# Kernel tuning notes

Hardware: AMD Instinct MI355X
Metric: run time of the kernel (lower is better)

## Reference

```python
import jax, jax.numpy as jnp
import numpy as np

S, B, H, E, V, L = 256, 32, 2000, 512, 10000, 6
EPS = 1e-5

def bn(x, g, b, m, v):
    # eval-mode batch norm over last (feature) dim
    return g * (x - m) * jax.lax.rsqrt(v + EPS) + b

def indrnn(x, u):
    # x: [S, B, F], u: [F]; h_t = relu(x_t + u * h_{t-1})
    def step(h, xt):
        h = jax.nn.relu(xt + u * h)
        return h, h
    h0 = jnp.zeros(x.shape[1:], x.dtype)
    _, ys = jax.lax.scan(step, h0, x)
    return ys

def setup_inputs():
    key = jax.random.key(0)
    ks = jax.random.split(key, 16)
    inp = {}
    inp['tokens'] = jax.random.randint(ks[0], (S, B), 0, V)
    inp['emb'] = jax.random.uniform(ks[1], (V, E), jnp.float32, -0.01, 0.01)
    inp['W0'] = jax.random.normal(ks[2], (E, H), jnp.float32) * (1.0 / np.sqrt(E))
    inp['b0'] = jnp.zeros((H,), jnp.float32)
    inp['Wr'] = jax.random.normal(ks[3], (L - 1, H, H), jnp.float32) * (1.0 / np.sqrt(H))
    inp['br'] = jnp.zeros((L - 1, H), jnp.float32)
    inp['u'] = jax.random.uniform(ks[4], (L, H), jnp.float32, 0.0, 1.0)
    inp['g'] = jnp.ones((L, H), jnp.float32)
    inp['be'] = jnp.zeros((L, H), jnp.float32)
    inp['mu'] = jnp.zeros((L, H), jnp.float32)
    inp['var'] = jnp.ones((L, H), jnp.float32)
    inp['Wl'] = jax.random.normal(ks[5], (H, E), jnp.float32) * (1.0 / np.sqrt(H))
    inp['bl'] = jnp.zeros((E,), jnp.float32)
    inp['ul'] = jax.random.uniform(ks[6], (E,), jnp.float32, 0.0, 1.0)
    inp['gl'] = jnp.ones((E,), jnp.float32)
    inp['bel'] = jnp.zeros((E,), jnp.float32)
    inp['mul'] = jnp.zeros((E,), jnp.float32)
    inp['varl'] = jnp.ones((E,), jnp.float32)
    inp['g2'] = jnp.ones((E,), jnp.float32)
    inp['be2'] = jnp.zeros((E,), jnp.float32)
    inp['mu2'] = jnp.zeros((E,), jnp.float32)
    inp['var2'] = jnp.ones((E,), jnp.float32)
    inp['Wd'] = jax.random.uniform(ks[7], (E, V), jnp.float32, -0.01, 0.01)
    inp['bd'] = jnp.zeros((V,), jnp.float32)
    return inp

def reference(tokens, emb, W0, b0, Wr, br, u, g, be, mu, var,
              Wl, bl, ul, gl, bel, mul, varl, g2, be2, mu2, var2, Wd, bd):
    x = emb[tokens]  # [S, B, E]
    # dropout layers are identity in eval mode
    for l in range(L):
        if l == 0:
            x = jnp.einsum('sbe,eh->sbh', x, W0) + b0
        else:
            x = jnp.einsum('sbh,hk->sbk', x, Wr[l - 1]) + br[l - 1]
        x = bn(x, g[l], be[l], mu[l], var[l])   # bn_before
        x = indrnn(x, u[l])
    x = jnp.einsum('sbh,he->sbe', x, Wl) + bl   # last_fc
    x = bn(x, gl, bel, mul, varl)
    x = indrnn(x, ul)                            # last_indrnn
    x = bn(x, g2, be2, mu2, var2)                # extra_bn (bn_before mode)
    out = (jnp.einsum('sbe,ev->sbv', x, Wd) + bd).reshape(S * B, V)
    return out
```

## Files before the change

kernel.cpp:

```cpp
#include <hip/hip_runtime.h>
#include <hip/hip_bf16.h>

#define S_LEN  256
#define BATCH  32
#define SB     8192
#define EDIM   512
#define HDIM   2000
#define HP     2048
#define VDIM   10000
#define VP     10240
#define EPS_BN 1e-5f


typedef __attribute__((ext_vector_type(8))) short bfx8;
typedef __attribute__((ext_vector_type(4))) float f32x4;

__device__ __forceinline__ void gload_lds16(const void* g, void* l) {
  __builtin_amdgcn_global_load_lds(
      (const __attribute__((address_space(1))) void*)g,
      (__attribute__((address_space(3))) void*)l, 16, 0, 0);
}

__device__ __forceinline__ float bf_lo(unsigned int w) {
  return __builtin_bit_cast(float, (unsigned int)(w << 16));
}
__device__ __forceinline__ float bf_hi(unsigned int w) {
  return __builtin_bit_cast(float, (unsigned int)(w & 0xFFFF0000u));
}
__device__ __forceinline__ unsigned int bf_pack(float lo, float hi) {
  unsigned short a = __builtin_bit_cast(unsigned short, __float2bfloat16(lo));
  unsigned short b = __builtin_bit_cast(unsigned short, __float2bfloat16(hi));
  return (unsigned int)a | ((unsigned int)b << 16);
}

#define PREP_GRID 29788
__global__ __launch_bounds__(256) void prep_kernel(
    const float* __restrict__ W0, const float* __restrict__ Wr,
    const float* __restrict__ Wl, const float* __restrict__ Wd,
    __hip_bfloat16* __restrict__ wt0, __hip_bfloat16* __restrict__ wtr,
    __hip_bfloat16* __restrict__ wtl, __hip_bfloat16* __restrict__ wtd,
    const float* __restrict__ b0, const float* __restrict__ br,
    const float* __restrict__ g,  const float* __restrict__ be,
    const float* __restrict__ mu, const float* __restrict__ var,
    const float* __restrict__ bl, const float* __restrict__ gl,
    const float* __restrict__ bel,const float* __restrict__ mul_,
    const float* __restrict__ varl,
    const float* __restrict__ g2, const float* __restrict__ be2,
    const float* __restrict__ mu2,const float* __restrict__ var2,
    const float* __restrict__ bd,
    float* es, float* eh, float* fs, float* fh,
    float* s2, float* h2, float* ds, float* dh,
    const int* __restrict__ tokens, const float* __restrict__ emb,
    __hip_bfloat16* __restrict__ xb) {
  __shared__ float tile[32][33];
  const int id = blockIdx.x;
  const int t = threadIdx.x;

  if (id < 27648) {
    const float* W; __hip_bfloat16* Wt; int K, N, Kp, Np, bx, by;
    if (id < 1024) {
      W = W0; Wt = wt0; K = EDIM; N = HDIM; Kp = EDIM; Np = HP;
      bx = id & 15; by = id >> 4;
    } else if (id < 21504) {
      int rel = id - 1024; int l = rel >> 12; int r2 = rel & 4095;
      W = Wr + (size_t)l * HDIM * HDIM; Wt = wtr + (size_t)l * HP * HP;
      K = HDIM; N = HDIM; Kp = HP; Np = HP;
      bx = r2 & 63; by = r2 >> 6;
    } else if (id < 22528) {
      int rel = id - 21504;
      W = Wl; Wt = wtl; K = HDIM; N = EDIM; Kp = HP; Np = EDIM;
      bx = rel & 63; by = rel >> 6;
    } else {
      int rel = id - 22528;
      W = Wd; Wt = wtd; K = EDIM; N = VDIM; Kp = EDIM; Np = VP;
      bx = rel & 15; by = rel >> 4;
    }
    const int tx = t & 31, ty = t >> 5;
    const int kb = bx * 32, nb = by * 32;
#pragma unroll
    for (int i = 0; i < 4; i++) {
      int k = kb + ty + i * 8, n = nb + tx;
      tile[ty + i * 8][tx] = (k < K && n < N) ? W[(size_t)k * N + n] : 0.f;
    }
    __syncthreads();
#pragma unroll
    for (int i = 0; i < 4; i++) {
      int n = nb + ty + i * 8, k = kb + tx;
      if (n < Np && k < Kp) Wt[(size_t)n * Kp + k] = __float2bfloat16(tile[tx][ty + i * 8]);
    }
    return;
  }

  if (id < 27740) {
    int tt = (id - 27648) * 256 + t;
    if (tt < 6 * HP) {
      int l = tt >> 11, h = tt & (HP - 1);
      float sc = 0.f, sh = 0.f;
      if (h < HDIM) {
        float s = g[l * HDIM + h] * rsqrtf(var[l * HDIM + h] + EPS_BN);
        float bias = (l == 0) ? b0[h] : br[(l - 1) * HDIM + h];
        sc = s;
        sh = (bias - mu[l * HDIM + h]) * s + be[l * HDIM + h];
      }
      es[tt] = sc; eh[tt] = sh;
      return;
    }
    tt -= 6 * HP;
    if (tt < EDIM) {
      float s = gl[tt] * rsqrtf(varl[tt] + EPS_BN);
      fs[tt] = s; fh[tt] = (bl[tt] - mul_[tt]) * s + bel[tt];
      return;
    }
    tt -= EDIM;
    if (tt < EDIM) {
      float s = g2[tt] * rsqrtf(var2[tt] + EPS_BN);
      s2[tt] = s; h2[tt] = be2[tt] - mu2[tt] * s;
      return;
    }
    tt -= EDIM;
    if (tt < VP) {
      ds[tt] = 1.f; dh[tt] = (tt < VDIM) ? bd[tt] : 0.f;
    }
    return;
  }

  {
    int idx = (id - 27740) * 256 + t;
    int mprime = idx >> 6;
    int e0 = (idx & 63) << 3;
    int s = mprime & 255, b = mprime >> 8;
    int tok = tokens[s * BATCH + b];
    const float* src = emb + (size_t)tok * EDIM + e0;
    float4 v0 = ((const float4*)src)[0];
    float4 v1 = ((const float4*)src)[1];
    __hip_bfloat16 tmp[8];
    tmp[0] = __float2bfloat16(v0.x); tmp[1] = __float2bfloat16(v0.y);
    tmp[2] = __float2bfloat16(v0.z); tmp[3] = __float2bfloat16(v0.w);
    tmp[4] = __float2bfloat16(v1.x); tmp[5] = __float2bfloat16(v1.y);
    tmp[6] = __float2bfloat16(v1.z); tmp[7] = __float2bfloat16(v1.w);
    *(bfx8*)&xb[(size_t)mprime * EDIM + e0] = *(const bfx8*)tmp;
  }
}

#define BARX  __builtin_amdgcn_s_barrier()
#define SP1   __builtin_amdgcn_s_setprio(1)
#define SP0   __builtin_amdgcn_s_setprio(0)
#define LGKM0 do { asm volatile("s_waitcnt lgkmcnt(0)" ::: "memory"); \
                   __builtin_amdgcn_sched_barrier(0); } while (0)
#define VMC(n) asm volatile("s_waitcnt vmcnt(" #n ")" ::: "memory")

__global__ __launch_bounds__(512, 2) void gemm256p_bf16_kernel(
    const __hip_bfloat16* __restrict__ A, int lda,
    const __hip_bfloat16* __restrict__ Bt, int ldb,
    __hip_bfloat16* __restrict__ Cb, float* __restrict__ Cf, int ldc,
    const float* __restrict__ epS, const float* __restrict__ epH,
    const float* __restrict__ uscan,
    int Kp, int Nstore, int grid_m, int chunk2d) {
  __shared__ __align__(16) char smem[131072];
  const int t = threadIdx.x, lane = t & 63, wid = t >> 6;
  const int nwg = gridDim.x, q = nwg >> 3, wg = blockIdx.x;
  int bm, bn;
  if (chunk2d) {
    const int xc = wg & 7, i = wg >> 3;
    bm = xc * 4 + (i >> 3);
    bn = i & 7;
  } else {
    const int swzb = (wg & 7) * q + (wg >> 3);
    bm = swzb % grid_m; bn = swzb / grid_m;
  }
  const int m0 = bm * 256, n0 = bn * 256;
  const int wm = wid >> 2, wn = wid & 3;

  const int lrow = lane >> 3;
  const int lch  = ((lane & 7) ^ lrow) * 8;
  const __hip_bfloat16* gA = A  + (size_t)(m0 + wid * 8 + lrow) * lda + lch;
  const __hip_bfloat16* gB = Bt + (size_t)(n0 + (wid >> 2) * 64 + (wid & 3) * 8 + lrow) * ldb + lch;
  char* const ldsA = (char*)smem;
  char* const ldsB = (char*)smem + 65536;
  const int laoff = wid * 1024;
  const int lboff = (wid >> 2) * 8192 + (wid & 3) * 1024;

#define STA(buf, e, kt) do {                                                   \
    gload_lds16(gA + (size_t)((e) * 64) * lda + (kt) * 64,                     \
                ldsA + (buf) * 32768 + (e) * 8192 + laoff);                    \
    gload_lds16(gA + (size_t)(128 + (e) * 64) * lda + (kt) * 64,               \
                ldsA + (buf) * 32768 + 16384 + (e) * 8192 + laoff);            \
  } while (0)
#define STB(buf, o, kt) do {                                                   \
    gload_lds16(gB + (size_t)((o) * 32) * ldb + (kt) * 64,                     \
                ldsB + (buf) * 32768 + (o) * 4096 + lboff);                    \
    gload_lds16(gB + (size_t)(128 + (o) * 32) * ldb + (kt) * 64,               \
                ldsB + (buf) * 32768 + 16384 + (o) * 4096 + lboff);            \
  } while (0)

  const int fr = lane & 15, cc = lane >> 4;
  const int sz = (fr & 7) << 4;
  const int ak0 = (cc * 16) ^ sz;
  const int ak1 = (64 + cc * 16) ^ sz;
  const char* rA = (char*)smem + (wm * 128 + fr) * 128;
  const char* rB = (char*)smem + 65536 + (wn * 64 + fr) * 128;

#define RDA(dst, buf, qa) do {                                                 \
    _Pragma("unroll") for (int mi = 0; mi < 4; mi++) {                         \
      dst[mi][0] = *(const bfx8*)(rA + (buf) * 32768 + (qa) * 8192 + mi * 2048 + ak0); \
      dst[mi][1] = *(const bfx8*)(rA + (buf) * 32768 + (qa) * 8192 + mi * 2048 + ak1); \
    } } while (0)
#define RDB(dst, buf, qb) do {                                                 \
    _Pragma("unroll") for (int nf = 0; nf < 2; nf++) {                         \
      dst[nf][0] = *(const bfx8*)(rB + (buf) * 32768 + (qb) * 4096 + nf * 2048 + ak0); \
      dst[nf][1] = *(const bfx8*)(rB + (buf) * 32768 + (qb) * 4096 + nf * 2048 + ak1); \
    } } while (0)
#define MM(qa, qb, aa, bb) do {                                                \
    _Pragma("unroll") for (int mi = 0; mi < 4; mi++)                           \
    _Pragma("unroll") for (int nf = 0; nf < 2; nf++)                           \
    _Pragma("unroll") for (int kk = 0; kk < 2; kk++)                           \
      acc[(qa) * 4 + mi][(qb) * 2 + nf] = __builtin_amdgcn_mfma_f32_16x16x32_bf16( \
          aa[mi][kk], bb[nf][kk], acc[(qa) * 4 + mi][(qb) * 2 + nf], 0, 0, 0); \
  } while (0)

  f32x4 acc[8][4];
#pragma unroll
  for (int i = 0; i < 8; i++)
#pragma unroll
    for (int j = 0; j < 4; j++) acc[i][j] = (f32x4){0.f, 0.f, 0.f, 0.f};

  const int NT = Kp >> 6;
  const int NI = NT >> 1;

  STA(0, 0, 0); STB(0, 0, 0); STB(0, 1, 0); STA(0, 1, 0);
  STA(1, 0, 1); STB(1, 0, 1);
  VMC(4); BARX;

  bfx8 a[4][2], b0[2][2], b2[2][2];
  for (int it = 0; it < NI - 1; ++it) {
    const int kt1 = 2 * it + 1, t2 = 2 * it + 2, t3 = 2 * it + 3;
    RDA(a, 0, 0); RDB(b0, 0, 0); STB(1, 1, kt1);
    BARX; LGKM0; SP1; MM(0, 0, a, b0); SP0; BARX;
    RDB(b2, 0, 1); STA(1, 1, kt1);
    BARX; LGKM0; SP1; MM(0, 1, a, b2); SP0; VMC(6); BARX;
    RDA(a, 0, 1); STA(0, 0, t2);
    BARX; LGKM0; SP1; MM(1, 0, a, b0); SP0; BARX;
    STB(0, 0, t2);
    BARX; LGKM0; SP1; MM(1, 1, a, b2); SP0; VMC(6); BARX;
    RDA(a, 1, 0); RDB(b0, 1, 0); STB(0, 1, t2);
    BARX; LGKM0; SP1; MM(0, 0, a, b0); SP0; BARX;
    RDB(b2, 1, 1); STA(0, 1, t2);
    BARX; LGKM0; SP1; MM(0, 1, a, b2); SP0; VMC(6); BARX;
    RDA(a, 1, 1); STA(1, 0, t3);
    BARX; LGKM0; SP1; MM(1, 0, a, b0); SP0; BARX;
    STB(1, 0, t3);
    BARX; LGKM0; SP1; MM(1, 1, a, b2); SP0; VMC(6); BARX;
  }
  {
    const int kt1 = NT - 1;
    RDA(a, 0, 0); RDB(b0, 0, 0); STB(1, 1, kt1);
    BARX; LGKM0; SP1; MM(0, 0, a, b0); SP0; BARX;
    RDB(b2, 0, 1); STA(1, 1, kt1);
    BARX; LGKM0; SP1; MM(0, 1, a, b2); SP0; VMC(6); BARX;
    RDA(a, 0, 1);
    BARX; LGKM0; SP1; MM(1, 0, a, b0); SP0; BARX;
    BARX; LGKM0; SP1; MM(1, 1, a, b2); SP0; VMC(2); BARX;
    RDA(a, 1, 0); RDB(b0, 1, 0);
    BARX; LGKM0; SP1; MM(0, 0, a, b0); SP0; BARX;
    RDB(b2, 1, 1);
    BARX; LGKM0; SP1; MM(0, 1, a, b2); SP0; VMC(0); BARX;
    RDA(a, 1, 1);
    BARX; LGKM0; SP1; MM(1, 0, a, b0); SP0; BARX;
    BARX; LGKM0; SP1; MM(1, 1, a, b2); SP0; BARX;
  }
  VMC(0);

  const int colb = n0 + wn * 64 + fr;
  const int rowb = wm * 128 + cc * 4;

  if (uscan) {
    unsigned short* lds16 = (unsigned short*)smem;
    const int colL0 = wn * 64 + fr;
#pragma unroll
    for (int nf = 0; nf < 4; nf++) {
      int colL = colL0 + nf * 16;
      float sc = epS[n0 + colL], sh = epH[n0 + colL];
#pragma unroll
      for (int mf = 0; mf < 8; mf++) {
#pragma unroll
        for (int rr = 0; rr < 4; rr++) {
          int s = rowb + mf * 16 + rr;
          int byte = ((s << 9) + (colL << 1)) ^ (((s >> 2) & 3) << 5);
          lds16[byte >> 1] = __builtin_bit_cast(unsigned short,
              __float2bfloat16(acc[mf][nf][rr] * sc + sh));
        }
      }
    }
    __syncthreads();
    if (t < 256) {
      const int c = t;
      const float uu = (n0 + c < HDIM) ? uscan[n0 + c] : 0.f;
      float h = 0.f;
      __hip_bfloat16* xcol = Cb + (size_t)m0 * ldc + n0 + c;
      for (int s8 = 0; s8 < 256; s8 += 8) {
        unsigned short vv[8];
#pragma unroll
        for (int j = 0; j < 8; j++) {
          int s = s8 + j;
          int byte = ((s << 9) + (c << 1)) ^ (((s >> 2) & 3) << 5);
          vv[j] = lds16[byte >> 1];
        }
#pragma unroll
        for (int j = 0; j < 8; j++) {
          h = fmaxf(fmaf(uu, h, bf_lo((unsigned int)vv[j])), 0.f);
          xcol[(size_t)(s8 + j) * ldc] = __float2bfloat16(h);
        }
      }
    }
    return;
  }

#pragma unroll
  for (int nf = 0; nf < 4; nf++) {
    int col = colb + nf * 16;
    if (col >= Nstore) continue;
    float sc = epS[col], sh = epH[col];
    if (Cf) {
#pragma unroll
      for (int mf = 0; mf < 8; mf++)
#pragma unroll
        for (int rr = 0; rr < 4; rr++) {
          int s = rowb + mf * 16 + rr;
          Cf[(size_t)(s * BATCH + bm) * ldc + col] = acc[mf][nf][rr] * sc + sh;
        }
    } else {
#pragma unroll
      for (int mf = 0; mf < 8; mf++)
#pragma unroll
        for (int rr = 0; rr < 4; rr++)
          Cb[(size_t)(m0 + rowb + mf * 16 + rr) * ldc + col] =
              __float2bfloat16(acc[mf][nf][rr] * sc + sh);
    }
  }
}

__global__ __launch_bounds__(256, 2) void gemm128_bf16_kernel(
    const __hip_bfloat16* __restrict__ A, int lda,
    const __hip_bfloat16* __restrict__ Bt, int ldb,
    __hip_bfloat16* __restrict__ C, int ldc,
    const float* __restrict__ epS, const float* __restrict__ epH,
    int Kp, int Nstore) {
  __shared__ __align__(16) __hip_bfloat16 As[128 * 32];
  __shared__ __align__(16) __hip_bfloat16 Bs[128 * 32];
  const int t = threadIdx.x;
  const int lane = t & 63;
  const int wave = t >> 6;
  const int m0 = blockIdx.x * 128;
  const int n0 = blockIdx.y * 128;
  const int wm = (wave >> 1) * 64;
  const int wn = (wave & 1) * 64;

  f32x4 acc[4][4];
#pragma unroll
  for (int i = 0; i < 4; i++)
#pragma unroll
    for (int j = 0; j < 4; j++) acc[i][j] = (f32x4){0.f, 0.f, 0.f, 0.f};

  const int kc = (t & 3) * 8;
  for (int k0 = 0; k0 < Kp; k0 += 32) {
#pragma unroll
    for (int r = 0; r < 2; r++) {
      int row = (r * 256 + t) >> 2;
      gload_lds16(A  + (size_t)(m0 + row) * lda + k0 + kc, &As[(r * 256 + (wave << 6)) * 8]);
      gload_lds16(Bt + (size_t)(n0 + row) * ldb + k0 + kc, &Bs[(r * 256 + (wave << 6)) * 8]);
    }
    __syncthreads();

    bfx8 af[4], bfr[4];
    const int fr = lane & 15;
    const int ko = (lane >> 4) * 8;
#pragma unroll
    for (int f = 0; f < 4; f++) af[f]  = *(const bfx8*)&As[(wm + f * 16 + fr) * 32 + ko];
#pragma unroll
    for (int f = 0; f < 4; f++) bfr[f] = *(const bfx8*)&Bs[(wn + f * 16 + fr) * 32 + ko];
#pragma unroll
    for (int i = 0; i < 4; i++)
#pragma unroll
      for (int j = 0; j < 4; j++)
        acc[i][j] = __builtin_amdgcn_mfma_f32_16x16x32_bf16(af[i], bfr[j], acc[i][j], 0, 0, 0);
    __syncthreads();
  }

  const int colb = n0 + wn + (lane & 15);
  const int rowb = m0 + wm + ((lane >> 4) << 2);
#pragma unroll
  for (int j = 0; j < 4; j++) {
    int col = colb + j * 16;
    if (col >= Nstore) continue;
    float sc = epS[col], sh = epH[col];
#pragma unroll
    for (int i = 0; i < 4; i++)
#pragma unroll
      for (int r = 0; r < 4; r++)
        C[(size_t)(rowb + i * 16 + r) * ldc + col] =
            __float2bfloat16(acc[i][j][r] * sc + sh);
  }
}

__global__ __launch_bounds__(64) void scan_final_kernel(
    const __hip_bfloat16* __restrict__ y, const float* __restrict__ ul,
    const float* __restrict__ s2, const float* __restrict__ h2,
    __hip_bfloat16* __restrict__ xb) {
  const int t = blockIdx.x * 64 + threadIdx.x;
  const int e2 = t & (EDIM / 2 - 1);
  const int b  = t >> 8;
  const int e0 = e2 * 2;
  const float u0 = ul[e0], u1 = ul[e0 + 1];
  const float sc0 = s2[e0], sh0 = h2[e0], sc1 = s2[e0 + 1], sh1 = h2[e0 + 1];
  const unsigned int* yp = (const unsigned int*)y;
  unsigned int* xp = (unsigned int*)xb;
  const size_t base0 = (size_t)b * 256 * (EDIM / 2) + e2;
  const size_t stride = EDIM / 2;
  float hv0 = 0.f, hv1 = 0.f;
  unsigned int q0[8], q1[8], q2[8], q3[8];
#define LD8(Q, bi) do { size_t o = base0 + (size_t)(bi) * 8 * stride;           \
    _Pragma("unroll") for (int j = 0; j < 8; j++) Q[j] = yp[o + (size_t)j * stride]; \
  } while (0)
#define PR8(Q, bi) do { size_t o = base0 + (size_t)(bi) * 8 * stride;           \
    _Pragma("unroll") for (int j = 0; j < 8; j++) {                             \
      hv0 = fmaxf(fmaf(u0, hv0, bf_lo(Q[j])), 0.f);                             \
      hv1 = fmaxf(fmaf(u1, hv1, bf_hi(Q[j])), 0.f);                             \
      xp[o + (size_t)j * stride] = bf_pack(hv0 * sc0 + sh0, hv1 * sc1 + sh1); } \
  } while (0)
  LD8(q0, 0); LD8(q1, 1); LD8(q2, 2);
  for (int c = 0; c < 32; c += 4) {
    LD8(q3, c + 3);
    PR8(q0, c);
    if (c + 4 < 32) LD8(q0, c + 4);
    PR8(q1, c + 1);
    if (c + 5 < 32) LD8(q1, c + 5);
    PR8(q2, c + 2);
    if (c + 6 < 32) LD8(q2, c + 6);
    PR8(q3, c + 3);
  }
#undef LD8
#undef PR8
}

extern "C" void kernel_launch(void* const* d_in, const int* in_sizes, int n_in,
                              void* d_out, int out_size, void* d_ws, size_t ws_size,
                              hipStream_t stream) {
  const int*   tokens = (const int*)d_in[0];
  const float* emb  = (const float*)d_in[1];
  const float* W0   = (const float*)d_in[2];
  const float* b0   = (const float*)d_in[3];
  const float* Wr   = (const float*)d_in[4];
  const float* br   = (const float*)d_in[5];
  const float* u    = (const float*)d_in[6];
  const float* g    = (const float*)d_in[7];
  const float* be   = (const float*)d_in[8];
  const float* mu   = (const float*)d_in[9];
  const float* var  = (const float*)d_in[10];
  const float* Wl   = (const float*)d_in[11];
  const float* bl   = (const float*)d_in[12];
  const float* ul   = (const float*)d_in[13];
  const float* gl   = (const float*)d_in[14];
  const float* bel  = (const float*)d_in[15];
  const float* mul_ = (const float*)d_in[16];
  const float* varl = (const float*)d_in[17];
  const float* g2   = (const float*)d_in[18];
  const float* be2  = (const float*)d_in[19];
  const float* mu2  = (const float*)d_in[20];
  const float* var2 = (const float*)d_in[21];
  const float* Wd   = (const float*)d_in[22];
  const float* bd   = (const float*)d_in[23];
  float* out = (float*)d_out;

  char* w = (char*)d_ws;
  auto carve = [&](size_t bytes) { void* p = (void*)w; w += (bytes + 255) & ~(size_t)255; return p; };
  __hip_bfloat16* wt0 = (__hip_bfloat16*)carve((size_t)HP * EDIM * 2);
  __hip_bfloat16* wtr = (__hip_bfloat16*)carve((size_t)5 * HP * HP * 2);
  __hip_bfloat16* wtl = (__hip_bfloat16*)carve((size_t)EDIM * HP * 2);
  __hip_bfloat16* wtd = (__hip_bfloat16*)carve((size_t)VP * EDIM * 2);
  __hip_bfloat16* xb  = (__hip_bfloat16*)carve((size_t)SB * HP * 2);
  __hip_bfloat16* xb2 = (__hip_bfloat16*)carve((size_t)SB * HP * 2);
  __hip_bfloat16* yb  = (__hip_bfloat16*)carve((size_t)SB * EDIM * 2);
  float* es  = (float*)carve((size_t)6 * HP * 4);
  float* eh  = (float*)carve((size_t)6 * HP * 4);
  float* fs  = (float*)carve((size_t)EDIM * 4);
  float* fh  = (float*)carve((size_t)EDIM * 4);
  float* s2b = (float*)carve((size_t)EDIM * 4);
  float* h2b = (float*)carve((size_t)EDIM * 4);
  float* dsb = (float*)carve((size_t)VP * 4);
  float* dhb = (float*)carve((size_t)VP * 4);

  prep_kernel<<<PREP_GRID, 256, 0, stream>>>(
      W0, Wr, Wl, Wd, wt0, wtr, wtl, wtd,
      b0, br, g, be, mu, var, bl, gl, bel, mul_, varl,
      g2, be2, mu2, var2, bd,
      es, eh, fs, fh, s2b, h2b, dsb, dhb,
      tokens, emb, xb);

  __hip_bfloat16* src = xb;
  __hip_bfloat16* dst = xb2;
  gemm256p_bf16_kernel<<<(SB / 256) * (HP / 256), 512, 0, stream>>>(
      src, EDIM, wt0, EDIM, dst, nullptr, HP, es, eh, u, EDIM, HP, SB / 256, 1);
  { __hip_bfloat16* tmp = src; src = dst; dst = tmp; }
  for (int l = 1; l < 6; l++) {
    gemm256p_bf16_kernel<<<(SB / 256) * (HP / 256), 512, 0, stream>>>(
        src, HP, wtr + (size_t)(l - 1) * HP * HP, HP, dst, nullptr, HP,
        es + l * HP, eh + l * HP, u + (size_t)l * HDIM, HP, HP, SB / 256, 1);
    __hip_bfloat16* tmp = src; src = dst; dst = tmp;
  }

  gemm128_bf16_kernel<<<dim3(SB / 128, EDIM / 128), 256, 0, stream>>>(
      src, HP, wtl, HP, yb, EDIM, fs, fh, HP, EDIM);
  scan_final_kernel<<<BATCH * EDIM / 2 / 64, 64, 0, stream>>>(yb, ul, s2b, h2b, dst);

  gemm256p_bf16_kernel<<<(SB / 256) * (VP / 256), 512, 0, stream>>>(
      dst, EDIM, wtd, EDIM, nullptr, out, VDIM, dsb, dhb, nullptr, EDIM, VDIM, SB / 256, 0);
}
```

Before: 598.8 us.

## Switch GEMM to triple-buffered K=32 LDS pipeline and split scan epilogue

The bf16 GEMM mainloop moves from a double-buffered K=64 tile layout to a three-stage ring of K=32 tiles, prefetching two tiles ahead. It uses a new swizzle and 96KB of LDS instead of 128KB. Because the scan epilogue no longer has room to stage all 256 rows, it now stages and scans the two 128-row halves one after the other, carrying the recurrence state between them. The goal is deeper load/compute overlap and a smaller LDS footprint. The cost is twice as many barrier-separated phases per unit of K, plus extra epilogue syncs.

```diff
diff --git a/kernel.cpp b/kernel.cpp
--- a/kernel.cpp
+++ b/kernel.cpp
@@ -156,7 +156,7 @@
     const float* __restrict__ epS, const float* __restrict__ epH,
     const float* __restrict__ uscan,
     int Kp, int Nstore, int grid_m, int chunk2d) {
-  __shared__ __align__(16) char smem[131072];
+  __shared__ __align__(16) char smem[98304];
   const int t = threadIdx.x, lane = t & 63, wid = t >> 6;
   const int nwg = gridDim.x, q = nwg >> 3, wg = blockIdx.x;
   int bm, bn;
@@ -171,104 +171,78 @@
   const int m0 = bm * 256, n0 = bn * 256;
   const int wm = wid >> 2, wn = wid & 3;
 
-  const int lrow = lane >> 3;
-  const int lch  = ((lane & 7) ^ lrow) * 8;
-  const __hip_bfloat16* gA = A  + (size_t)(m0 + wid * 8 + lrow) * lda + lch;
-  const __hip_bfloat16* gB = Bt + (size_t)(n0 + (wid >> 2) * 64 + (wid & 3) * 8 + lrow) * ldb + lch;
+  const int srow = lane >> 2;
+  const int sch  = ((lane & 3) ^ (srow & 3)) * 8;
+  const __hip_bfloat16* gA2 = A  + (size_t)(m0 + wid * 16 + srow) * lda + sch;
+  const __hip_bfloat16* gB2 = Bt + (size_t)(n0 + wid * 16 + srow) * ldb + sch;
   char* const ldsA = (char*)smem;
-  char* const ldsB = (char*)smem + 65536;
-  const int laoff = wid * 1024;
-  const int lboff = (wid >> 2) * 8192 + (wid & 3) * 1024;
-
-#define STA(buf, e, kt) do {                                                   \
-    gload_lds16(gA + (size_t)((e) * 64) * lda + (kt) * 64,                     \
-                ldsA + (buf) * 32768 + (e) * 8192 + laoff);                    \
-    gload_lds16(gA + (size_t)(128 + (e) * 64) * lda + (kt) * 64,               \
-                ldsA + (buf) * 32768 + 16384 + (e) * 8192 + laoff);            \
+  char* const ldsB = (char*)smem + 49152;
+
+#define STA32(buf, e, kt) \
+  gload_lds16(gA2 + (size_t)(e) * 128 * lda + (kt) * 32, \
+              ldsA + (buf) * 16384 + (e) * 8192 + wid * 1024)
+#define STB32(buf, o, kt) \
+  gload_lds16(gB2 + (size_t)(o) * 128 * ldb + (kt) * 32, \
+              ldsB + (buf) * 16384 + (o) * 8192 + wid * 1024)
+
+  const int fr = lane & 15, cc = lane >> 4;
+  const int xo = (cc ^ (fr & 3)) << 4;
+  const char* rA32 = (char*)smem + (wm * 128 + fr) * 64 + xo;
+  const char* rB32 = (char*)smem + 49152 + wn * 4096 + fr * 64 + xo;
+
+#define RDA32(dst, bb, qa) do {                                               \
+    _Pragma("unroll") for (int mi = 0; mi < 4; mi++)                          \
+      dst[mi] = *(const bfx8*)(rA32 + (bb) * 16384 + (qa) * 4096 + mi * 1024);\
   } while (0)
-#define STB(buf, o, kt) do {                                                   \
-    gload_lds16(gB + (size_t)((o) * 32) * ldb + (kt) * 64,                     \
-                ldsB + (buf) * 32768 + (o) * 4096 + lboff);                    \
-    gload_lds16(gB + (size_t)(128 + (o) * 32) * ldb + (kt) * 64,               \
-                ldsB + (buf) * 32768 + 16384 + (o) * 4096 + lboff);            \
+#define RDB32(dst, bb, qb) do {                                               \
+    _Pragma("unroll") for (int nf = 0; nf < 2; nf++)                          \
+      dst[nf] = *(const bfx8*)(rB32 + (bb) * 16384 + (qb) * 2048 + nf * 1024);\
   } while (0)
-
-  const int fr = lane & 15, cc = lane >> 4;
-  const int sz = (fr & 7) << 4;
-  const int ak0 = (cc * 16) ^ sz;
-  const int ak1 = (64 + cc * 16) ^ sz;
-  const char* rA = (char*)smem + (wm * 128 + fr) * 128;
-  const char* rB = (char*)smem + 65536 + (wn * 64 + fr) * 128;
-
-#define RDA(dst, buf, qa) do {                                                 \
-    _Pragma("unroll") for (int mi = 0; mi < 4; mi++) {                         \
-      dst[mi][0] = *(const bfx8*)(rA + (buf) * 32768 + (qa) * 8192 + mi * 2048 + ak0); \
-      dst[mi][1] = *(const bfx8*)(rA + (buf) * 32768 + (qa) * 8192 + mi * 2048 + ak1); \
-    } } while (0)
-#define RDB(dst, buf, qb) do {                                                 \
-    _Pragma("unroll") for (int nf = 0; nf < 2; nf++) {                         \
-      dst[nf][0] = *(const bfx8*)(rB + (buf) * 32768 + (qb) * 4096 + nf * 2048 + ak0); \
-      dst[nf][1] = *(const bfx8*)(rB + (buf) * 32768 + (qb) * 4096 + nf * 2048 + ak1); \
-    } } while (0)
-#define MM(qa, qb, aa, bb) do {                                                \
-    _Pragma("unroll") for (int mi = 0; mi < 4; mi++)                           \
-    _Pragma("unroll") for (int nf = 0; nf < 2; nf++)                           \
-    _Pragma("unroll") for (int kk = 0; kk < 2; kk++)                           \
-      acc[(qa) * 4 + mi][(qb) * 2 + nf] = __builtin_amdgcn_mfma_f32_16x16x32_bf16( \
-          aa[mi][kk], bb[nf][kk], acc[(qa) * 4 + mi][(qb) * 2 + nf], 0, 0, 0); \
+#define MM32(qa, qb, aa, bb) do {                                             \
+    _Pragma("unroll") for (int mi = 0; mi < 4; mi++)                          \
+    _Pragma("unroll") for (int nf = 0; nf < 2; nf++)                          \
+      acc[(qa) * 4 + mi][(qb) * 2 + nf] =                                     \
+          __builtin_amdgcn_mfma_f32_16x16x32_bf16(                            \
+              aa[mi], bb[nf], acc[(qa) * 4 + mi][(qb) * 2 + nf], 0, 0, 0);    \
   } while (0)
 
+#define TILE32(bt, st, kt2, DOSTAGE, ENDWAIT) do {                            \
+    RDA32(a, bt, 0); RDB32(b0, bt, 0); if (DOSTAGE) STA32(st, 0, kt2);        \
+    BARX; LGKM0; SP1; MM32(0, 0, a, b0); SP0; BARX;                           \
+    RDB32(b2, bt, 1); if (DOSTAGE) STB32(st, 0, kt2);                         \
+    BARX; LGKM0; SP1; MM32(0, 1, a, b2); SP0; BARX;                           \
+    RDA32(a, bt, 1); if (DOSTAGE) STA32(st, 1, kt2);                          \
+    BARX; LGKM0; SP1; MM32(1, 0, a, b0); SP0; BARX;                           \
+    if (DOSTAGE) STB32(st, 1, kt2);                                           \
+    BARX; LGKM0; SP1; MM32(1, 1, a, b2); SP0; ENDWAIT; BARX;                  \
+  } while (0)
+
   f32x4 acc[8][4];
 #pragma unroll
   for (int i = 0; i < 8; i++)
 #pragma unroll
     for (int j = 0; j < 4; j++) acc[i][j] = (f32x4){0.f, 0.f, 0.f, 0.f};
 
-  const int NT = Kp >> 6;
-  const int NI = NT >> 1;
-
-  STA(0, 0, 0); STB(0, 0, 0); STB(0, 1, 0); STA(0, 1, 0);
-  STA(1, 0, 1); STB(1, 0, 1);
+  const int NT = Kp >> 5;
+
+  STA32(0, 0, 0); STB32(0, 0, 0); STA32(0, 1, 0); STB32(0, 1, 0);
+  STA32(1, 0, 1); STB32(1, 0, 1); STA32(1, 1, 1); STB32(1, 1, 1);
   VMC(4); BARX;
 
-  bfx8 a[4][2], b0[2][2], b2[2][2];
-  for (int it = 0; it < NI - 1; ++it) {
-    const int kt1 = 2 * it + 1, t2 = 2 * it + 2, t3 = 2 * it + 3;
-    RDA(a, 0, 0); RDB(b0, 0, 0); STB(1, 1, kt1);
-    BARX; LGKM0; SP1; MM(0, 0, a, b0); SP0; BARX;
-    RDB(b2, 0, 1); STA(1, 1, kt1);
-    BARX; LGKM0; SP1; MM(0, 1, a, b2); SP0; VMC(6); BARX;
-    RDA(a, 0, 1); STA(0, 0, t2);
-    BARX; LGKM0; SP1; MM(1, 0, a, b0); SP0; BARX;
-    STB(0, 0, t2);
-    BARX; LGKM0; SP1; MM(1, 1, a, b2); SP0; VMC(6); BARX;
-    RDA(a, 1, 0); RDB(b0, 1, 0); STB(0, 1, t2);
-    BARX; LGKM0; SP1; MM(0, 0, a, b0); SP0; BARX;
-    RDB(b2, 1, 1); STA(0, 1, t2);
-    BARX; LGKM0; SP1; MM(0, 1, a, b2); SP0; VMC(6); BARX;
-    RDA(a, 1, 1); STA(1, 0, t3);
-    BARX; LGKM0; SP1; MM(1, 0, a, b0); SP0; BARX;
-    STB(1, 0, t3);
-    BARX; LGKM0; SP1; MM(1, 1, a, b2); SP0; VMC(6); BARX;
+  bfx8 a[4], b0[2], b2[2];
+  int bt = 0;
+  for (int kt = 0; kt < NT - 2; ++kt) {
+    int st = bt + 2; if (st >= 3) st -= 3;
+    TILE32(bt, st, kt + 2, true, VMC(4));
+    bt = (bt + 1 == 3) ? 0 : bt + 1;
   }
   {
-    const int kt1 = NT - 1;
-    RDA(a, 0, 0); RDB(b0, 0, 0); STB(1, 1, kt1);
-    BARX; LGKM0; SP1; MM(0, 0, a, b0); SP0; BARX;
-    RDB(b2, 0, 1); STA(1, 1, kt1);
-    BARX; LGKM0; SP1; MM(0, 1, a, b2); SP0; VMC(6); BARX;
-    RDA(a, 0, 1);
-    BARX; LGKM0; SP1; MM(1, 0, a, b0); SP0; BARX;
-    BARX; LGKM0; SP1; MM(1, 1, a, b2); SP0; VMC(2); BARX;
-    RDA(a, 1, 0); RDB(b0, 1, 0);
-    BARX; LGKM0; SP1; MM(0, 0, a, b0); SP0; BARX;
-    RDB(b2, 1, 1);
-    BARX; LGKM0; SP1; MM(0, 1, a, b2); SP0; VMC(0); BARX;
-    RDA(a, 1, 1);
-    BARX; LGKM0; SP1; MM(1, 0, a, b0); SP0; BARX;
-    BARX; LGKM0; SP1; MM(1, 1, a, b2); SP0; BARX;
-  }
-  VMC(0);
+    TILE32(bt, 0, 0, false, VMC(0));
+    bt = (bt + 1 == 3) ? 0 : bt + 1;
+  }
+  {
+    TILE32(bt, 0, 0, false, (void)0);
+  }
 
   const int colb = n0 + wn * 64 + fr;
   const int rowb = wm * 128 + cc * 4;
@@ -276,28 +250,30 @@
   if (uscan) {
     unsigned short* lds16 = (unsigned short*)smem;
     const int colL0 = wn * 64 + fr;
-#pragma unroll
-    for (int nf = 0; nf < 4; nf++) {
-      int colL = colL0 + nf * 16;
-      float sc = epS[n0 + colL], sh = epH[n0 + colL];
-#pragma unroll
-      for (int mf = 0; mf < 8; mf++) {
-#pragma unroll
-        for (int rr = 0; rr < 4; rr++) {
-          int s = rowb + mf * 16 + rr;
-          int byte = ((s << 9) + (colL << 1)) ^ (((s >> 2) & 3) << 5);
-          lds16[byte >> 1] = __builtin_bit_cast(unsigned short,
-              __float2bfloat16(acc[mf][nf][rr] * sc + sh));
-        }
+    if (wm == 0) {
+#pragma unroll
+      for (int nf = 0; nf < 4; nf++) {
+        int colL = colL0 + nf * 16;
+        float sc = epS[n0 + colL], sh = epH[n0 + colL];
+#pragma unroll
+        for (int mf = 0; mf < 8; mf++)
+#pragma unroll
+          for (int rr = 0; rr < 4; rr++) {
+            int s = cc * 4 + mf * 16 + rr;
+            int byte = ((s << 9) + (colL << 1)) ^ (((s >> 2) & 3) << 5);
+            lds16[byte >> 1] = __builtin_bit_cast(unsigned short,
+                __float2bfloat16(acc[mf][nf][rr] * sc + sh));
+          }
       }
     }
     __syncthreads();
+    float hrun = 0.f, uu = 0.f;
+    __hip_bfloat16* xcol = nullptr;
+    const int c = t;
     if (t < 256) {
-      const int c = t;
-      const float uu = (n0 + c < HDIM) ? uscan[n0 + c] : 0.f;
-      float h = 0.f;
-      __hip_bfloat16* xcol = Cb + (size_t)m0 * ldc + n0 + c;
-      for (int s8 = 0; s8 < 256; s8 += 8) {
+      uu = (n0 + c < HDIM) ? uscan[n0 + c] : 0.f;
+      xcol = Cb + (size_t)m0 * ldc + n0 + c;
+      for (int s8 = 0; s8 < 128; s8 += 8) {
         unsigned short vv[8];
 #pragma unroll
         for (int j = 0; j < 8; j++) {
@@ -307,8 +283,42 @@
         }
 #pragma unroll
         for (int j = 0; j < 8; j++) {
-          h = fmaxf(fmaf(uu, h, bf_lo((unsigned int)vv[j])), 0.f);
-          xcol[(size_t)(s8 + j) * ldc] = __float2bfloat16(h);
+          hrun = fmaxf(fmaf(uu, hrun, bf_lo((unsigned int)vv[j])), 0.f);
+          xcol[(size_t)(s8 + j) * ldc] = __float2bfloat16(hrun);
+        }
+      }
+    }
+    __syncthreads();
+    if (wm == 1) {
+#pragma unroll
+      for (int nf = 0; nf < 4; nf++) {
+        int colL = colL0 + nf * 16;
+        float sc = epS[n0 + colL], sh = epH[n0 + colL];
+#pragma unroll
+        for (int mf = 0; mf < 8; mf++)
+#pragma unroll
+          for (int rr = 0; rr < 4; rr++) {
+            int s = cc * 4 + mf * 16 + rr;
+            int byte = ((s << 9) + (colL << 1)) ^ (((s >> 2) & 3) << 5);
+            lds16[byte >> 1] = __builtin_bit_cast(unsigned short,
+                __float2bfloat16(acc[mf][nf][rr] * sc + sh));
+          }
+      }
+    }
+    __syncthreads();
+    if (t < 256) {
+      for (int s8 = 0; s8 < 128; s8 += 8) {
+        unsigned short vv[8];
+#pragma unroll
+        for (int j = 0; j < 8; j++) {
+          int s = s8 + j;
+          int byte = ((s << 9) + (c << 1)) ^ (((s >> 2) & 3) << 5);
+          vv[j] = lds16[byte >> 1];
+        }
+#pragma unroll
+        for (int j = 0; j < 8; j++) {
+          hrun = fmaxf(fmaf(uu, hrun, bf_lo((unsigned int)vv[j])), 0.f);
+          xcol[(size_t)(128 + s8 + j) * ldc] = __float2bfloat16(hrun);
         }
       }
     }
```

Measured after the change: 686.9 us. 14.7% more time.

## Fuse six layer GEMM+scan launches into one cooperative persistent kernel

Applied to the files above, without the earlier changes.

Replaces the six separate per-layer GEMM+IndRNN-scan kernel launches with a single cooperative kernel of 256 workgroups that loops over the layers, using grid.sync between them. A fallback path keeps the old multi-launch sequence if the cooperative launch fails. The aim is to remove launch gaps and tail effects between layers, at the cost of a grid-wide barrier and a fixed grid that needs all blocks co-resident. The final-projection epilogue is also reordered so the row loop sits outside the column loop, to make the fp32 stores better coalesced.

```diff
diff --git a/kernel.cpp b/kernel.cpp
--- a/kernel.cpp
+++ b/kernel.cpp
@@ -1,5 +1,8 @@
 #include <hip/hip_runtime.h>
 #include <hip/hip_bf16.h>
+#include <hip/hip_cooperative_groups.h>
+
+namespace cg = cooperative_groups;
 
 #define S_LEN  256
 #define BATCH  32
@@ -149,37 +152,6 @@
                    __builtin_amdgcn_sched_barrier(0); } while (0)
 #define VMC(n) asm volatile("s_waitcnt vmcnt(" #n ")" ::: "memory")
 
-__global__ __launch_bounds__(512, 2) void gemm256p_bf16_kernel(
-    const __hip_bfloat16* __restrict__ A, int lda,
-    const __hip_bfloat16* __restrict__ Bt, int ldb,
-    __hip_bfloat16* __restrict__ Cb, float* __restrict__ Cf, int ldc,
-    const float* __restrict__ epS, const float* __restrict__ epH,
-    const float* __restrict__ uscan,
-    int Kp, int Nstore, int grid_m, int chunk2d) {
-  __shared__ __align__(16) char smem[131072];
-  const int t = threadIdx.x, lane = t & 63, wid = t >> 6;
-  const int nwg = gridDim.x, q = nwg >> 3, wg = blockIdx.x;
-  int bm, bn;
-  if (chunk2d) {
-    const int xc = wg & 7, i = wg >> 3;
-    bm = xc * 4 + (i >> 3);
-    bn = i & 7;
-  } else {
-    const int swzb = (wg & 7) * q + (wg >> 3);
-    bm = swzb % grid_m; bn = swzb / grid_m;
-  }
-  const int m0 = bm * 256, n0 = bn * 256;
-  const int wm = wid >> 2, wn = wid & 3;
-
-  const int lrow = lane >> 3;
-  const int lch  = ((lane & 7) ^ lrow) * 8;
-  const __hip_bfloat16* gA = A  + (size_t)(m0 + wid * 8 + lrow) * lda + lch;
-  const __hip_bfloat16* gB = Bt + (size_t)(n0 + (wid >> 2) * 64 + (wid & 3) * 8 + lrow) * ldb + lch;
-  char* const ldsA = (char*)smem;
-  char* const ldsB = (char*)smem + 65536;
-  const int laoff = wid * 1024;
-  const int lboff = (wid >> 2) * 8192 + (wid & 3) * 1024;
-
 #define STA(buf, e, kt) do {                                                   \
     gload_lds16(gA + (size_t)((e) * 64) * lda + (kt) * 64,                     \
                 ldsA + (buf) * 32768 + (e) * 8192 + laoff);                    \
@@ -192,14 +164,6 @@
     gload_lds16(gB + (size_t)(128 + (o) * 32) * ldb + (kt) * 64,               \
                 ldsB + (buf) * 32768 + 16384 + (o) * 4096 + lboff);            \
   } while (0)
-
-  const int fr = lane & 15, cc = lane >> 4;
-  const int sz = (fr & 7) << 4;
-  const int ak0 = (cc * 16) ^ sz;
-  const int ak1 = (64 + cc * 16) ^ sz;
-  const char* rA = (char*)smem + (wm * 128 + fr) * 128;
-  const char* rB = (char*)smem + 65536 + (wn * 64 + fr) * 128;
-
 #define RDA(dst, buf, qa) do {                                                 \
     _Pragma("unroll") for (int mi = 0; mi < 4; mi++) {                         \
       dst[mi][0] = *(const bfx8*)(rA + (buf) * 32768 + (qa) * 8192 + mi * 2048 + ak0); \
@@ -218,6 +182,184 @@
           aa[mi][kk], bb[nf][kk], acc[(qa) * 4 + mi][(qb) * 2 + nf], 0, 0, 0); \
   } while (0)
 
+#define KLOOP(NTv) do {                                                        \
+    const int NI = (NTv) >> 1;                                                 \
+    STA(0, 0, 0); STB(0, 0, 0); STB(0, 1, 0); STA(0, 1, 0);                    \
+    STA(1, 0, 1); STB(1, 0, 1);                                                \
+    VMC(4); BARX;                                                              \
+    for (int it = 0; it < NI - 1; ++it) {                                      \
+      const int kt1 = 2 * it + 1, t2 = 2 * it + 2, t3 = 2 * it + 3;            \
+      RDA(a, 0, 0); RDB(b0, 0, 0); STB(1, 1, kt1);                             \
+      BARX; LGKM0; SP1; MM(0, 0, a, b0); SP0; BARX;                            \
+      RDB(b2, 0, 1); STA(1, 1, kt1);                                           \
+      BARX; LGKM0; SP1; MM(0, 1, a, b2); SP0; VMC(6); BARX;                    \
+      RDA(a, 0, 1); STA(0, 0, t2);                                             \
+      BARX; LGKM0; SP1; MM(1, 0, a, b0); SP0; BARX;                            \
+      STB(0, 0, t2);                                                           \
+      BARX; LGKM0; SP1; MM(1, 1, a, b2); SP0; VMC(6); BARX;                    \
+      RDA(a, 1, 0); RDB(b0, 1, 0); STB(0, 1, t2);                              \
+      BARX; LGKM0; SP1; MM(0, 0, a, b0); SP0; BARX;                            \
+      RDB(b2, 1, 1); STA(0, 1, t2);                                            \
+      BARX; LGKM0; SP1; MM(0, 1, a, b2); SP0; VMC(6); BARX;                    \
+      RDA(a, 1, 1); STA(1, 0, t3);                                             \
+      BARX; LGKM0; SP1; MM(1, 0, a, b0); SP0; BARX;                            \
+      STB(1, 0, t3);                                                           \
+      BARX; LGKM0; SP1; MM(1, 1, a, b2); SP0; VMC(6); BARX;                    \
+    }                                                                          \
+    {                                                                          \
+      const int kt1 = (NTv) - 1;                                               \
+      RDA(a, 0, 0); RDB(b0, 0, 0); STB(1, 1, kt1);                             \
+      BARX; LGKM0; SP1; MM(0, 0, a, b0); SP0; BARX;                            \
+      RDB(b2, 0, 1); STA(1, 1, kt1);                                           \
+      BARX; LGKM0; SP1; MM(0, 1, a, b2); SP0; VMC(6); BARX;                    \
+      RDA(a, 0, 1);                                                            \
+      BARX; LGKM0; SP1; MM(1, 0, a, b0); SP0; BARX;                            \
+      BARX; LGKM0; SP1; MM(1, 1, a, b2); SP0; VMC(2); BARX;                    \
+      RDA(a, 1, 0); RDB(b0, 1, 0);                                             \
+      BARX; LGKM0; SP1; MM(0, 0, a, b0); SP0; BARX;                            \
+      RDB(b2, 1, 1);                                                           \
+      BARX; LGKM0; SP1; MM(0, 1, a, b2); SP0; VMC(0); BARX;                    \
+      RDA(a, 1, 1);                                                            \
+      BARX; LGKM0; SP1; MM(1, 0, a, b0); SP0; BARX;                            \
+      BARX; LGKM0; SP1; MM(1, 1, a, b2); SP0; BARX;                            \
+    }                                                                          \
+    VMC(0);                                                                    \
+  } while (0)
+
+__global__ __launch_bounds__(512, 2) void layers6_kernel(
+    __hip_bfloat16* __restrict__ xb, __hip_bfloat16* __restrict__ xb2,
+    const __hip_bfloat16* __restrict__ wt0, const __hip_bfloat16* __restrict__ wtr,
+    const float* __restrict__ es, const float* __restrict__ eh,
+    const float* __restrict__ u) {
+  cg::grid_group grid = cg::this_grid();
+  __shared__ __align__(16) char smem[131072];
+  const int t = threadIdx.x, lane = t & 63, wid = t >> 6;
+  const int wg = blockIdx.x;
+  const int xc = wg & 7, ii = wg >> 3;
+  const int bm = xc * 4 + (ii >> 3);
+  const int bn = ii & 7;
+  const int m0 = bm * 256, n0 = bn * 256;
+  const int wm = wid >> 2, wn = wid & 3;
+
+  const int lrow = lane >> 3;
+  const int lch  = ((lane & 7) ^ lrow) * 8;
+  char* const ldsA = (char*)smem;
+  char* const ldsB = (char*)smem + 65536;
+  const int laoff = wid * 1024;
+  const int lboff = (wid >> 2) * 8192 + (wid & 3) * 1024;
+  const int fr = lane & 15, cc = lane >> 4;
+  const int sz = (fr & 7) << 4;
+  const int ak0 = (cc * 16) ^ sz;
+  const int ak1 = (64 + cc * 16) ^ sz;
+  const char* rA = (char*)smem + (wm * 128 + fr) * 128;
+  const char* rB = (char*)smem + 65536 + (wn * 64 + fr) * 128;
+  const int rowb = wm * 128 + cc * 4;
+
+  for (int l = 0; l < 6; ++l) {
+    const __hip_bfloat16* A = (l & 1) ? xb2 : xb;
+    __hip_bfloat16* C = (l & 1) ? xb : xb2;
+    const int lda = l ? HP : EDIM;
+    const int ldb = lda;
+    const __hip_bfloat16* Bt = l ? wtr + (size_t)(l - 1) * HP * HP : wt0;
+    const float* epS = es + l * HP;
+    const float* epH = eh + l * HP;
+    const float* uscan = u + (size_t)l * HDIM;
+    const int NT = lda >> 6;
+
+    const __hip_bfloat16* gA = A  + (size_t)(m0 + wid * 8 + lrow) * lda + lch;
+    const __hip_bfloat16* gB = Bt + (size_t)(n0 + (wid >> 2) * 64 + (wid & 3) * 8 + lrow) * ldb + lch;
+
+    f32x4 acc[8][4];
+#pragma unroll
+    for (int i = 0; i < 8; i++)
+#pragma unroll
+      for (int j = 0; j < 4; j++) acc[i][j] = (f32x4){0.f, 0.f, 0.f, 0.f};
+
+    bfx8 a[4][2], b0[2][2], b2[2][2];
+    KLOOP(NT);
+
+    {
+      unsigned short* lds16 = (unsigned short*)smem;
+      const int colL0 = wn * 64 + fr;
+#pragma unroll
+      for (int nf = 0; nf < 4; nf++) {
+        int colL = colL0 + nf * 16;
+        float sc = epS[n0 + colL], sh = epH[n0 + colL];
+#pragma unroll
+        for (int mf = 0; mf < 8; mf++) {
+#pragma unroll
+          for (int rr = 0; rr < 4; rr++) {
+            int s = rowb + mf * 16 + rr;
+            int byte = ((s << 9) + (colL << 1)) ^ (((s >> 2) & 3) << 5);
+            lds16[byte >> 1] = __builtin_bit_cast(unsigned short,
+                __float2bfloat16(acc[mf][nf][rr] * sc + sh));
+          }
+        }
+      }
+      __syncthreads();
+      if (t < 256) {
+        const int c = t;
+        const float uu = (n0 + c < HDIM) ? uscan[n0 + c] : 0.f;
+        float h = 0.f;
+        __hip_bfloat16* xcol = C + (size_t)m0 * HP + n0 + c;
+        for (int s8 = 0; s8 < 256; s8 += 8) {
+          unsigned short vv[8];
+#pragma unroll
+          for (int j = 0; j < 8; j++) {
+            int s = s8 + j;
+            int byte = ((s << 9) + (c << 1)) ^ (((s >> 2) & 3) << 5);
+            vv[j] = lds16[byte >> 1];
+          }
+#pragma unroll
+          for (int j = 0; j < 8; j++) {
+            h = fmaxf(fmaf(uu, h, bf_lo((unsigned int)vv[j])), 0.f);
+            xcol[(size_t)(s8 + j) * HP] = __float2bfloat16(h);
+          }
+        }
+      }
+    }
+    __threadfence();
+    grid.sync();
+  }
+}
+
+__global__ __launch_bounds__(512, 2) void gemm256p_bf16_kernel(
+    const __hip_bfloat16* __restrict__ A, int lda,
+    const __hip_bfloat16* __restrict__ Bt, int ldb,
+    __hip_bfloat16* __restrict__ Cb, float* __restrict__ Cf, int ldc,
+    const float* __restrict__ epS, const float* __restrict__ epH,
+    const float* __restrict__ uscan,
+    int Kp, int Nstore, int grid_m, int chunk2d) {
+  __shared__ __align__(16) char smem[131072];
+  const int t = threadIdx.x, lane = t & 63, wid = t >> 6;
+  const int nwg = gridDim.x, q = nwg >> 3, wg = blockIdx.x;
+  int bm, bn;
+  if (chunk2d) {
+    const int xc = wg & 7, ii = wg >> 3;
+    bm = xc * 4 + (ii >> 3);
+    bn = ii & 7;
+  } else {
+    const int swzb = (wg & 7) * q + (wg >> 3);
+    bm = swzb % grid_m; bn = swzb / grid_m;
+  }
+  const int m0 = bm * 256, n0 = bn * 256;
+  const int wm = wid >> 2, wn = wid & 3;
+
+  const int lrow = lane >> 3;
+  const int lch  = ((lane & 7) ^ lrow) * 8;
+  const __hip_bfloat16* gA = A  + (size_t)(m0 + wid * 8 + lrow) * lda + lch;
+  const __hip_bfloat16* gB = Bt + (size_t)(n0 + (wid >> 2) * 64 + (wid & 3) * 8 + lrow) * ldb + lch;
+  char* const ldsA = (char*)smem;
+  char* const ldsB = (char*)smem + 65536;
+  const int laoff = wid * 1024;
+  const int lboff = (wid >> 2) * 8192 + (wid & 3) * 1024;
+  const int fr = lane & 15, cc = lane >> 4;
+  const int sz = (fr & 7) << 4;
+  const int ak0 = (cc * 16) ^ sz;
+  const int ak1 = (64 + cc * 16) ^ sz;
+  const char* rA = (char*)smem + (wm * 128 + fr) * 128;
+  const char* rB = (char*)smem + 65536 + (wn * 64 + fr) * 128;
+
   f32x4 acc[8][4];
 #pragma unroll
   for (int i = 0; i < 8; i++)
@@ -225,50 +367,8 @@
     for (int j = 0; j < 4; j++) acc[i][j] = (f32x4){0.f, 0.f, 0.f, 0.f};
 
   const int NT = Kp >> 6;
-  const int NI = NT >> 1;
-
-  STA(0, 0, 0); STB(0, 0, 0); STB(0, 1, 0); STA(0, 1, 0);
-  STA(1, 0, 1); STB(1, 0, 1);
-  VMC(4); BARX;
-
   bfx8 a[4][2], b0[2][2], b2[2][2];
-  for (int it = 0; it < NI - 1; ++it) {
-    const int kt1 = 2 * it + 1, t2 = 2 * it + 2, t3 = 2 * it + 3;
-    RDA(a, 0, 0); RDB(b0, 0, 0); STB(1, 1, kt1);
-    BARX; LGKM0; SP1; MM(0, 0, a, b0); SP0; BARX;
-    RDB(b2, 0, 1); STA(1, 1, kt1);
-    BARX; LGKM0; SP1; MM(0, 1, a, b2); SP0; VMC(6); BARX;
-    RDA(a, 0, 1); STA(0, 0, t2);
-    BARX; LGKM0; SP1; MM(1, 0, a, b0); SP0; BARX;
-    STB(0, 0, t2);
-    BARX; LGKM0; SP1; MM(1, 1, a, b2); SP0; VMC(6); BARX;
-    RDA(a, 1, 0); RDB(b0, 1, 0); STB(0, 1, t2);
-    BARX; LGKM0; SP1; MM(0, 0, a, b0); SP0; BARX;
-    RDB(b2, 1, 1); STA(0, 1, t2);
-    BARX; LGKM0; SP1; MM(0, 1, a, b2); SP0; VMC(6); BARX;
-    RDA(a, 1, 1); STA(1, 0, t3);
-    BARX; LGKM0; SP1; MM(1, 0, a, b0); SP0; BARX;
-    STB(1, 0, t3);
-    BARX; LGKM0; SP1; MM(1, 1, a, b2); SP0; VMC(6); BARX;
-  }
-  {
-    const int kt1 = NT - 1;
-    RDA(a, 0, 0); RDB(b0, 0, 0); STB(1, 1, kt1);
-    BARX; LGKM0; SP1; MM(0, 0, a, b0); SP0; BARX;
-    RDB(b2, 0, 1); STA(1, 1, kt1);
-    BARX; LGKM0; SP1; MM(0, 1, a, b2); SP0; VMC(6); BARX;
-    RDA(a, 0, 1);
-    BARX; LGKM0; SP1; MM(1, 0, a, b0); SP0; BARX;
-    BARX; LGKM0; SP1; MM(1, 1, a, b2); SP0; VMC(2); BARX;
-    RDA(a, 1, 0); RDB(b0, 1, 0);
-    BARX; LGKM0; SP1; MM(0, 0, a, b0); SP0; BARX;
-    RDB(b2, 1, 1);
-    BARX; LGKM0; SP1; MM(0, 1, a, b2); SP0; VMC(0); BARX;
-    RDA(a, 1, 1);
-    BARX; LGKM0; SP1; MM(1, 0, a, b0); SP0; BARX;
-    BARX; LGKM0; SP1; MM(1, 1, a, b2); SP0; BARX;
-  }
-  VMC(0);
+  KLOOP(NT);
 
   const int colb = n0 + wn * 64 + fr;
   const int rowb = wm * 128 + cc * 4;
@@ -315,20 +415,35 @@
     return;
   }
 
-#pragma unroll
-  for (int nf = 0; nf < 4; nf++) {
-    int col = colb + nf * 16;
-    if (col >= Nstore) continue;
-    float sc = epS[col], sh = epH[col];
-    if (Cf) {
-#pragma unroll
-      for (int mf = 0; mf < 8; mf++)
-#pragma unroll
-        for (int rr = 0; rr < 4; rr++) {
-          int s = rowb + mf * 16 + rr;
-          Cf[(size_t)(s * BATCH + bm) * ldc + col] = acc[mf][nf][rr] * sc + sh;
+  if (Cf) {
+    float scv[4], shv[4];
+#pragma unroll
+    for (int nf = 0; nf < 4; nf++) {
+      int col = colb + nf * 16;
+      bool ok = col < Nstore;
+      scv[nf] = ok ? epS[col] : 0.f;
+      shv[nf] = ok ? epH[col] : 0.f;
+    }
+#pragma unroll
+    for (int mf = 0; mf < 8; mf++) {
+#pragma unroll
+      for (int rr = 0; rr < 4; rr++) {
+        int s = rowb + mf * 16 + rr;
+        size_t rb = (size_t)(s * BATCH + bm) * ldc;
+#pragma unroll
+        for (int nf = 0; nf < 4; nf++) {
+          int col = colb + nf * 16;
+          if (col < Nstore)
+            Cf[rb + col] = acc[mf][nf][rr] * scv[nf] + shv[nf];
         }
-    } else {
+      }
+    }
+  } else {
+#pragma unroll
+    for (int nf = 0; nf < 4; nf++) {
+      int col = colb + nf * 16;
+      if (col >= Nstore) continue;
+      float sc = epS[col], sh = epH[col];
 #pragma unroll
       for (int mf = 0; mf < 8; mf++)
 #pragma unroll
@@ -496,22 +611,33 @@
       es, eh, fs, fh, s2b, h2b, dsb, dhb,
       tokens, emb, xb);
 
-  __hip_bfloat16* src = xb;
-  __hip_bfloat16* dst = xb2;
-  gemm256p_bf16_kernel<<<(SB / 256) * (HP / 256), 512, 0, stream>>>(
-      src, EDIM, wt0, EDIM, dst, nullptr, HP, es, eh, u, EDIM, HP, SB / 256, 1);
-  { __hip_bfloat16* tmp = src; src = dst; dst = tmp; }
-  for (int l = 1; l < 6; l++) {
-    gemm256p_bf16_kernel<<<(SB / 256) * (HP / 256), 512, 0, stream>>>(
-        src, HP, wtr + (size_t)(l - 1) * HP * HP, HP, dst, nullptr, HP,
-        es + l * HP, eh + l * HP, u + (size_t)l * HDIM, HP, HP, SB / 256, 1);
-    __hip_bfloat16* tmp = src; src = dst; dst = tmp;
+  {
+    __hip_bfloat16* xbp = xb; __hip_bfloat16* xb2p = xb2;
+    const __hip_bfloat16* wt0p = wt0; const __hip_bfloat16* wtrp = wtr;
+    const float* esp = es; const float* ehp = eh; const float* up = u;
+    void* args[] = {&xbp, &xb2p, &wt0p, &wtrp, &esp, &ehp, &up};
+    hipError_t rc = hipLaunchCooperativeKernel(
+        (const void*)layers6_kernel, dim3(256), dim3(512), args, 0, stream);
+    if (rc != hipSuccess) {
+      (void)hipGetLastError();
+      __hip_bfloat16* src = xb;
+      __hip_bfloat16* dst = xb2;
+      gemm256p_bf16_kernel<<<256, 512, 0, stream>>>(
+          src, EDIM, wt0, EDIM, dst, nullptr, HP, es, eh, u, EDIM, HP, SB / 256, 1);
+      { __hip_bfloat16* tmp = src; src = dst; dst = tmp; }
+      for (int l = 1; l < 6; l++) {
+        gemm256p_bf16_kernel<<<256, 512, 0, stream>>>(
+            src, HP, wtr + (size_t)(l - 1) * HP * HP, HP, dst, nullptr, HP,
+            es + l * HP, eh + l * HP, u + (size_t)l * HDIM, HP, HP, SB / 256, 1);
+        __hip_bfloat16* tmp = src; src = dst; dst = tmp;
+      }
+    }
   }
 
   gemm128_bf16_kernel<<<dim3(SB / 128, EDIM / 128), 256, 0, stream>>>(
-      src, HP, wtl, HP, yb, EDIM, fs, fh, HP, EDIM);
-  scan_final_kernel<<<BATCH * EDIM / 2 / 64, 64, 0, stream>>>(yb, ul, s2b, h2b, dst);
+      xb, HP, wtl, HP, yb, EDIM, fs, fh, HP, EDIM);
+  scan_final_kernel<<<BATCH * EDIM / 2 / 64, 64, 0, stream>>>(yb, ul, s2b, h2b, xb2);
 
   gemm256p_bf16_kernel<<<(SB / 256) * (VP / 256), 512, 0, stream>>>(
-      dst, EDIM, wtd, EDIM, nullptr, out, VDIM, dsb, dhb, nullptr, EDIM, VDIM, SB / 256, 0);
-}
+      xb2, EDIM, wtd, EDIM, nullptr, out, VDIM, dsb, dhb, nullptr, EDIM, VDIM, SB / 256, 0);
+}
```

Result: slower. 1.248 ms (+108.4%).
